# Optimization experiments

Measured on AMD Instinct MI355X. Metric: run time of the kernel, lower is better.

The kernel has to match this reference:

```python
import jax, jax.numpy as jnp
import numpy as np

N = 12000       # num nodes
E = 384000      # num edges (avg degree 32)
F_IN = 512      # num_feats
H = 64          # gnn_hid_dim (== anchor_dim)
C = 7           # num_cls
SIGMA = 1.0


def setup_inputs() -> dict:
    key = jax.random.key(0)
    ks = jax.random.split(key, 9)
    scale = lambda fan_in: 1.0 / np.sqrt(fan_in)
    return {
        "x": jax.random.normal(ks[0], (N, F_IN), dtype=jnp.float32),
        "W1": jax.random.normal(ks[1], (F_IN, H), dtype=jnp.float32) * scale(F_IN),
        "b1": jnp.zeros((H,), dtype=jnp.float32),
        "W2": jax.random.normal(ks[2], (H, H), dtype=jnp.float32) * scale(H),
        "b2": jnp.zeros((H,), dtype=jnp.float32),
        "aux": jax.random.normal(ks[3], (H,), dtype=jnp.float32),
        "clf_W": jax.random.normal(ks[4], (2 * H, C), dtype=jnp.float32) * scale(2 * H),
        "clf_b": jnp.zeros((C,), dtype=jnp.float32),
        "edge_index": jax.random.randint(ks[5], (2, E), 0, N, dtype=jnp.int64),
    }


def gcn_conv(x, W, b, src, dst, n):
    # GCNConv: D^{-1/2} (A + I) D^{-1/2} X W + b, with self-loops
    h = x @ W                                                   # [N, out]
    deg = jax.ops.segment_sum(jnp.ones(src.shape[0], h.dtype), dst,
                              num_segments=n) + 1.0             # +1 for self-loop
    inv_sqrt = jax.lax.rsqrt(deg)
    norm = inv_sqrt[src] * inv_sqrt[dst]                        # [E]
    agg = jax.ops.segment_sum(h[src] * norm[:, None], dst, num_segments=n)
    agg = agg + h / deg[:, None]                                # self-loop term (norm = 1/deg)
    return agg + b


def reference(x, W1, b1, W2, b2, aux, clf_W, clf_b, edge_index):
    src, dst = edge_index[0], edge_index[1]
    n = x.shape[0]
    h = jax.nn.relu(gcn_conv(x, W1, b1, src, dst, n))
    h = gcn_conv(h, W2, b2, src, dst, n)                        # [N, H]
    # kernel aggregate: pairwise Gaussian kernel on cosine scores
    a = aux / jnp.maximum(jnp.linalg.norm(aux), 1e-12)          # F.normalize
    hn = jnp.maximum(jnp.linalg.norm(h, axis=-1), 1e-8)         # cosine_similarity eps
    score = (h @ a) / hn                                        # [N]
    diff = score[None, :] - score[:, None]                      # [N, N]
    kappa = jnp.exp(-(diff * diff) / (SIGMA * SIGMA))           # [N, N]
    z = (kappa @ h) / jnp.sum(kappa, axis=1, keepdims=True)     # [N, H]
    return jnp.concatenate([h, z], axis=-1) @ clf_W + clf_b     # [N, C]
```

## Files before the change

kernel.cpp:

```cpp
#include <hip/hip_runtime.h>
#include <hip/hip_bf16.h>

#define N_NODES 12000
#define N_EDGES 384000
#define F_IN 512
#define H 64
#define C_CLS 7
#define KTERMS 16
#define PAD 96
#define CSTR 32
#define MOM_BLKS 192
#define NB 4
#define GEMM_BLKS 188
#define FILL_BLKS 256
#define XS_STR 68

__device__ __forceinline__ float wred_f(float x) {
    #pragma unroll
    for (int o = 32; o > 0; o >>= 1) x += __shfl_xor(x, o);
    return x;
}

__global__ __launch_bounds__(256) void init_k(int* __restrict__ cur,
                                              double* __restrict__ M,
                                              double* __restrict__ m0) {
    int i = blockIdx.x * 256 + threadIdx.x;
    if (i < N_NODES) cur[i * CSTR] = 0;
    if (i < KTERMS * 64) M[i] = 0.0;
    if (i < KTERMS) m0[i] = 0.0;
}

__global__ __launch_bounds__(256) void k1_gemm_fill(const float* __restrict__ x,
                                                    const float* __restrict__ W1,
                                                    const int* __restrict__ ei,
                                                    float* __restrict__ hbuf,
                                                    int* __restrict__ cur,
                                                    int* __restrict__ csrc) {
    const int b = blockIdx.x, t = threadIdx.x;
    if (b < GEMM_BLKS) {
        __shared__ float xs[64 * XS_STR];
        __shared__ float wsm[64 * 64];
        const int tx = t & 15, ty = t >> 4;
        const int i0 = b * 64;
        float acc[4][4] = {};
        for (int k0 = 0; k0 < F_IN; k0 += 64) {
            #pragma unroll
            for (int q = 0; q < 4; ++q) {
                int idx = t + q * 256;
                int row = idx >> 4, kg = idx & 15;
                int rg = min(i0 + row, N_NODES - 1);
                *(float4*)(&xs[row * XS_STR + kg * 4]) =
                    *(const float4*)(x + (size_t)rg * F_IN + k0 + kg * 4);
            }
            #pragma unroll
            for (int q = 0; q < 4; ++q) {
                int idx = t + q * 256;
                int r = idx >> 4, cg = idx & 15;
                *(float4*)(&wsm[r * 64 + cg * 4]) =
                    *(const float4*)(W1 + (size_t)(k0 + r) * H + cg * 4);
            }
            __syncthreads();
            #pragma unroll
            for (int kk0 = 0; kk0 < 64; kk0 += 4) {
                float4 a0 = *(const float4*)(&xs[(ty * 4 + 0) * XS_STR + kk0]);
                float4 a1 = *(const float4*)(&xs[(ty * 4 + 1) * XS_STR + kk0]);
                float4 a2 = *(const float4*)(&xs[(ty * 4 + 2) * XS_STR + kk0]);
                float4 a3 = *(const float4*)(&xs[(ty * 4 + 3) * XS_STR + kk0]);
                float4 b0 = *(const float4*)(&wsm[(kk0 + 0) * 64 + tx * 4]);
                float4 b1 = *(const float4*)(&wsm[(kk0 + 1) * 64 + tx * 4]);
                float4 b2 = *(const float4*)(&wsm[(kk0 + 2) * 64 + tx * 4]);
                float4 b3 = *(const float4*)(&wsm[(kk0 + 3) * 64 + tx * 4]);
                #define MAC4(AV, BV) \
                    acc[0][0] += AV.x * BV.x; acc[0][1] += AV.x * BV.y; \
                    acc[0][2] += AV.x * BV.z; acc[0][3] += AV.x * BV.w;
                acc[0][0] += a0.x * b0.x; acc[0][1] += a0.x * b0.y; acc[0][2] += a0.x * b0.z; acc[0][3] += a0.x * b0.w;
                acc[0][0] += a0.y * b1.x; acc[0][1] += a0.y * b1.y; acc[0][2] += a0.y * b1.z; acc[0][3] += a0.y * b1.w;
                acc[0][0] += a0.z * b2.x; acc[0][1] += a0.z * b2.y; acc[0][2] += a0.z * b2.z; acc[0][3] += a0.z * b2.w;
                acc[0][0] += a0.w * b3.x; acc[0][1] += a0.w * b3.y; acc[0][2] += a0.w * b3.z; acc[0][3] += a0.w * b3.w;
                acc[1][0] += a1.x * b0.x; acc[1][1] += a1.x * b0.y; acc[1][2] += a1.x * b0.z; acc[1][3] += a1.x * b0.w;
                acc[1][0] += a1.y * b1.x; acc[1][1] += a1.y * b1.y; acc[1][2] += a1.y * b1.z; acc[1][3] += a1.y * b1.w;
                acc[1][0] += a1.z * b2.x; acc[1][1] += a1.z * b2.y; acc[1][2] += a1.z * b2.z; acc[1][3] += a1.z * b2.w;
                acc[1][0] += a1.w * b3.x; acc[1][1] += a1.w * b3.y; acc[1][2] += a1.w * b3.z; acc[1][3] += a1.w * b3.w;
                acc[2][0] += a2.x * b0.x; acc[2][1] += a2.x * b0.y; acc[2][2] += a2.x * b0.z; acc[2][3] += a2.x * b0.w;
                acc[2][0] += a2.y * b1.x; acc[2][1] += a2.y * b1.y; acc[2][2] += a2.y * b1.z; acc[2][3] += a2.y * b1.w;
                acc[2][0] += a2.z * b2.x; acc[2][1] += a2.z * b2.y; acc[2][2] += a2.z * b2.z; acc[2][3] += a2.z * b2.w;
                acc[2][0] += a2.w * b3.x; acc[2][1] += a2.w * b3.y; acc[2][2] += a2.w * b3.z; acc[2][3] += a2.w * b3.w;
                acc[3][0] += a3.x * b0.x; acc[3][1] += a3.x * b0.y; acc[3][2] += a3.x * b0.z; acc[3][3] += a3.x * b0.w;
                acc[3][0] += a3.y * b1.x; acc[3][1] += a3.y * b1.y; acc[3][2] += a3.y * b1.z; acc[3][3] += a3.y * b1.w;
                acc[3][0] += a3.z * b2.x; acc[3][1] += a3.z * b2.y; acc[3][2] += a3.z * b2.z; acc[3][3] += a3.z * b2.w;
                acc[3][0] += a3.w * b3.x; acc[3][1] += a3.w * b3.y; acc[3][2] += a3.w * b3.z; acc[3][3] += a3.w * b3.w;
                #undef MAC4
            }
            __syncthreads();
        }
        #pragma unroll
        for (int r = 0; r < 4; ++r) {
            int row = i0 + ty * 4 + r;
            if (row < N_NODES)
                *(float4*)(hbuf + (size_t)row * H + tx * 4) =
                    make_float4(acc[r][0], acc[r][1], acc[r][2], acc[r][3]);
        }
    } else {
        for (int e = (b - GEMM_BLKS) * 256 + t; e < N_EDGES; e += FILL_BLKS * 256) {
            int s = ei[e];
            int d = ei[N_EDGES + e];
            int pos = atomicAdd(&cur[d * CSTR], 1);
            if (pos < PAD) csrc[d * PAD + pos] = s;
        }
    }
}

__global__ __launch_bounds__(256) void agg1_k(const float* __restrict__ hbuf,
                                              const float* __restrict__ b1,
                                              const int* __restrict__ cur,
                                              const int* __restrict__ csrc,
                                              float* __restrict__ h1) {
    __shared__ int2 sPair[NB * PAD];
    __shared__ int sDeg[NB];
    __shared__ float sIsd[NB];
    const int t = threadIdx.x, f = t & 63, w = t >> 6;
    const int base = blockIdx.x * NB;
    if (t < NB) {
        int d = cur[(base + t) * CSTR];
        sDeg[t] = min(d, PAD);
        sIsd[t] = rsqrtf((float)d + 1.f);
    }
    __syncthreads();
    for (int idx = t; idx < NB * PAD; idx += 256) {
        int n = idx / PAD, e = idx - n * PAD;
        if (e < sDeg[n]) {
            int s = csrc[(base + n) * PAD + e];
            float ws_ = rsqrtf((float)cur[s * CSTR] + 1.f);
            sPair[idx] = make_int2(s, __float_as_int(ws_));
        }
    }
    __syncthreads();
    const int i = base + w;
    const int deg = sDeg[w];
    const float isd = sIsd[w];
    const int2* pp = sPair + w * PAD;
    float acc = 0.f;
    int e = 0;
    for (; e + 4 <= deg; e += 4) {
        int2 p0 = pp[e], p1 = pp[e + 1], p2 = pp[e + 2], p3 = pp[e + 3];
        acc += hbuf[p0.x * H + f] * __int_as_float(p0.y)
             + hbuf[p1.x * H + f] * __int_as_float(p1.y)
             + hbuf[p2.x * H + f] * __int_as_float(p2.y)
             + hbuf[p3.x * H + f] * __int_as_float(p3.y);
    }
    for (; e < deg; ++e) {
        int2 p = pp[e];
        acc += hbuf[p.x * H + f] * __int_as_float(p.y);
    }
    float res = (acc + hbuf[i * H + f] * isd) * isd + b1[f];
    h1[i * H + f] = fmaxf(res, 0.f);
}

__global__ __launch_bounds__(256) void agg2_k(const float* __restrict__ h1,
                                              const float* __restrict__ W2,
                                              const float* __restrict__ b2,
                                              const float* __restrict__ aux,
                                              const int* __restrict__ cur,
                                              const int* __restrict__ csrc,
                                              float* __restrict__ h2,
                                              float* __restrict__ score) {
    __shared__ float w2s[64 * 64];
    __shared__ int2 sPair[NB * PAD];
    __shared__ int sDeg[NB];
    __shared__ float sIsd[NB];
    __shared__ float anorm[64];
    __shared__ float gsh[NB * 64];
    const int t = threadIdx.x, f = t & 63, w = t >> 6;
    const int base = blockIdx.x * NB;
    #pragma unroll
    for (int q = 0; q < 4; ++q) {
        int idx = t + q * 256;
        int r = idx >> 4, c4 = idx & 15;
        *(float4*)(&w2s[r * 64 + c4 * 4]) = *(const float4*)(W2 + r * H + c4 * 4);
    }
    if (t < NB) {
        int d = cur[(base + t) * CSTR];
        sDeg[t] = min(d, PAD);
        sIsd[t] = rsqrtf((float)d + 1.f);
    }
    if (t < 64) {
        float av = aux[t];
        anorm[t] = av * rsqrtf(fmaxf(wred_f(av * av), 1e-24f));
    }
    __syncthreads();
    for (int idx = t; idx < NB * PAD; idx += 256) {
        int n = idx / PAD, e = idx - n * PAD;
        if (e < sDeg[n]) {
            int s = csrc[(base + n) * PAD + e];
            float ws_ = rsqrtf((float)cur[s * CSTR] + 1.f);
            sPair[idx] = make_int2(s, __float_as_int(ws_));
        }
    }
    __syncthreads();
    const int i = base + w;
    const int deg = sDeg[w];
    const float isd = sIsd[w];
    const int2* pp = sPair + w * PAD;
    float acc = 0.f;
    int e = 0;
    for (; e + 4 <= deg; e += 4) {
        int2 p0 = pp[e], p1 = pp[e + 1], p2 = pp[e + 2], p3 = pp[e + 3];
        acc += h1[p0.x * H + f] * __int_as_float(p0.y)
             + h1[p1.x * H + f] * __int_as_float(p1.y)
             + h1[p2.x * H + f] * __int_as_float(p2.y)
             + h1[p3.x * H + f] * __int_as_float(p3.y);
    }
    for (; e < deg; ++e) {
        int2 p = pp[e];
        acc += h1[p.x * H + f] * __int_as_float(p.y);
    }
    float g = (acc + h1[i * H + f] * isd) * isd;
    gsh[w * 64 + f] = g;
    __builtin_amdgcn_wave_barrier();
    float hv = b2[f];
    #pragma unroll 16
    for (int k = 0; k < 64; ++k) hv += gsh[w * 64 + k] * w2s[k * 64 + f];
    h2[i * H + f] = hv;
    float dp = wred_f(hv * anorm[f]);
    float nn = wred_f(hv * hv);
    if (f == 0) score[i] = dp / fmaxf(sqrtf(nn), 1e-8f);
}

__global__ __launch_bounds__(256) void momden_k(const float* __restrict__ h2,
                                                const float* __restrict__ score,
                                                double* __restrict__ M,
                                                double* __restrict__ m0) {
    const int t = threadIdx.x, f = t & 63, g = t >> 6;
    float accM[KTERMS], accD[KTERMS];
    #pragma unroll
    for (int k = 0; k < KTERMS; ++k) { accM[k] = 0.f; accD[k] = 0.f; }
    for (int j = blockIdx.x * 4 + g; j < N_NODES; j += MOM_BLKS * 4) {
        float sj = score[j];
        float wj = expf(-sj * sj);
        float hv = h2[j * H + f];
        float tm = wj * hv, td = wj;
        #pragma unroll
        for (int k = 0; k < KTERMS; ++k) {
            accM[k] += tm; tm *= sj;
            accD[k] += td; td *= sj;
        }
    }
    __shared__ float Msh[4 * KTERMS * 64];
    __shared__ float Dsh[4 * KTERMS];
    #pragma unroll
    for (int k = 0; k < KTERMS; ++k) Msh[(g * KTERMS + k) * 64 + f] = accM[k];
    if (f == 0) {
        #pragma unroll
        for (int k = 0; k < KTERMS; ++k) Dsh[g * KTERMS + k] = accD[k];
    }
    __syncthreads();
    for (int idx = t; idx < KTERMS * 64; idx += 256) {
        int k = idx >> 6, ff = idx & 63;
        float sum = Msh[(0 * KTERMS + k) * 64 + ff] + Msh[(1 * KTERMS + k) * 64 + ff]
                  + Msh[(2 * KTERMS + k) * 64 + ff] + Msh[(3 * KTERMS + k) * 64 + ff];
        unsafeAtomicAdd(&M[idx], (double)sum);
    }
    if (t < KTERMS) {
        float sum = Dsh[t] + Dsh[KTERMS + t] + Dsh[2 * KTERMS + t] + Dsh[3 * KTERMS + t];
        unsafeAtomicAdd(&m0[t], (double)sum);
    }
}

__global__ __launch_bounds__(256) void final_k(const float* __restrict__ h2,
                                               const float* __restrict__ score,
                                               const double* __restrict__ M,
                                               const double* __restrict__ m0,
                                               const float* __restrict__ clfW,
                                               const float* __restrict__ clfb,
                                               float* __restrict__ out) {
    __shared__ float Ms[KTERMS * 64];
    __shared__ float m0s[KTERMS];
    __shared__ float cw[128 * C_CLS];
    __shared__ float cb[8];
    __shared__ float zh[4 * 128];
    const int t = threadIdx.x, f = t & 63, w = t >> 6;
    for (int idx = t; idx < KTERMS * 64; idx += 256) Ms[idx] = (float)M[idx];
    if (t < KTERMS) m0s[t] = (float)m0[t];
    for (int idx = t; idx < 128 * C_CLS; idx += 256) cw[idx] = clfW[idx];
    if (t < C_CLS) cb[t] = clfb[t];
    __syncthreads();
    const int base = blockIdx.x * 16;
    for (int q = 0; q < 4; ++q) {
        int i = base + q * 4 + w;
        float s = score[i];
        float c = expf(-s * s);
        float t2 = 2.f * s;
        float num = 0.f, den = 0.f;
        #pragma unroll
        for (int k = 0; k < KTERMS; ++k) {
            num += c * Ms[k * 64 + f];
            den += c * m0s[k];
            c *= t2 * (1.0f / (float)(k + 1));
        }
        zh[w * 128 + f] = h2[i * H + f];
        zh[w * 128 + 64 + f] = num / den;
        __builtin_amdgcn_wave_barrier();
        if (f < C_CLS) {
            float o = cb[f];
            #pragma unroll 8
            for (int u = 0; u < 128; ++u) o += zh[w * 128 + u] * cw[u * C_CLS + f];
            out[(size_t)i * C_CLS + f] = o;
        }
        __builtin_amdgcn_wave_barrier();
    }
}

extern "C" void kernel_launch(void* const* d_in, const int* in_sizes, int n_in,
                              void* d_out, int out_size, void* d_ws, size_t ws_size,
                              hipStream_t stream) {
    (void)in_sizes; (void)n_in; (void)out_size; (void)ws_size;
    const float* x    = (const float*)d_in[0];
    const float* W1   = (const float*)d_in[1];
    const float* b1   = (const float*)d_in[2];
    const float* W2   = (const float*)d_in[3];
    const float* b2   = (const float*)d_in[4];
    const float* aux  = (const float*)d_in[5];
    const float* clfW = (const float*)d_in[6];
    const float* clfb = (const float*)d_in[7];
    const int*   ei   = (const int*)d_in[8];
    float* out = (float*)d_out;
    char* ws = (char*)d_ws;

    float*  hbuf  = (float*)(ws + 0);
    float*  h1    = (float*)(ws + 3072000);
    float*  h2    = (float*)(ws + 6144000);
    float*  score = (float*)(ws + 9216000);
    int*    csrc  = (int*)  (ws + 9264000);
    int*    cur   = (int*)  (ws + 13872000);
    double* M     = (double*)(ws + 15408000);
    double* m0    = (double*)(ws + 15416192);

    init_k<<<47, 256, 0, stream>>>(cur, M, m0);
    k1_gemm_fill<<<GEMM_BLKS + FILL_BLKS, 256, 0, stream>>>(x, W1, ei, hbuf, cur, csrc);
    agg1_k<<<N_NODES / NB, 256, 0, stream>>>(hbuf, b1, cur, csrc, h1);
    agg2_k<<<N_NODES / NB, 256, 0, stream>>>(h1, W2, b2, aux, cur, csrc, h2, score);
    momden_k<<<MOM_BLKS, 256, 0, stream>>>(h2, score, M, m0);
    final_k<<<750, 256, 0, stream>>>(h2, score, M, m0, clfW, clfb, out);
}
```

Before: 96.48 us.

## Fuse pipeline stages into persistent megakernel with software grid barriers

```diff
diff --git a/kernel.cpp b/kernel.cpp
--- a/kernel.cpp
+++ b/kernel.cpp
@@ -9,10 +9,11 @@
 #define KTERMS 16
 #define PAD 96
 #define CSTR 32
+#define NBLK 640
+#define GEMM_BLKS 188
+#define FILL_BLKS (NBLK - GEMM_BLKS)
 #define MOM_BLKS 192
 #define NB 4
-#define GEMM_BLKS 188
-#define FILL_BLKS 256
 #define XS_STR 68
 
 __device__ __forceinline__ float wred_f(float x) {
@@ -21,25 +22,62 @@
     return x;
 }
 
+__device__ __forceinline__ void stc(float* p, float v) {
+    __hip_atomic_store(p, v, __ATOMIC_RELAXED, __HIP_MEMORY_SCOPE_AGENT);
+}
+
+__device__ __forceinline__ void gsync(int* bar, int gen) {
+    __syncthreads();
+    if (threadIdx.x == 0) {
+        const int s = blockIdx.x & 7;
+        int pos = __hip_atomic_fetch_add(&bar[s * 32], 1, __ATOMIC_RELAXED,
+                                         __HIP_MEMORY_SCOPE_AGENT);
+        if (pos == 80 * gen - 1) {
+            int r = __hip_atomic_fetch_add(&bar[320], 1, __ATOMIC_RELAXED,
+                                           __HIP_MEMORY_SCOPE_AGENT);
+            if (r == 8 * gen - 1) {
+                #pragma unroll
+                for (int k = 0; k < 8; ++k)
+                    __hip_atomic_store(&bar[512 + k * 32], gen, __ATOMIC_RELAXED,
+                                       __HIP_MEMORY_SCOPE_AGENT);
+            }
+        }
+        while (__hip_atomic_load(&bar[512 + s * 32], __ATOMIC_RELAXED,
+                                 __HIP_MEMORY_SCOPE_AGENT) < gen)
+            __builtin_amdgcn_s_sleep(8);
+        asm volatile("" ::: "memory");
+    }
+    __syncthreads();
+}
+
 __global__ __launch_bounds__(256) void init_k(int* __restrict__ cur,
                                               double* __restrict__ M,
-                                              double* __restrict__ m0) {
+                                              double* __restrict__ m0,
+                                              int* __restrict__ bar) {
     int i = blockIdx.x * 256 + threadIdx.x;
     if (i < N_NODES) cur[i * CSTR] = 0;
     if (i < KTERMS * 64) M[i] = 0.0;
     if (i < KTERMS) m0[i] = 0.0;
-}
-
-__global__ __launch_bounds__(256) void k1_gemm_fill(const float* __restrict__ x,
-                                                    const float* __restrict__ W1,
-                                                    const int* __restrict__ ei,
-                                                    float* __restrict__ hbuf,
-                                                    int* __restrict__ cur,
-                                                    int* __restrict__ csrc) {
+    if (i < 768) bar[i] = 0;
+}
+
+__global__ __launch_bounds__(256, 4) void mega_k(
+        const float* __restrict__ x, const float* __restrict__ W1,
+        const float* __restrict__ b1, const float* __restrict__ W2,
+        const float* __restrict__ b2, const float* __restrict__ aux,
+        const float* __restrict__ clfW, const float* __restrict__ clfb,
+        const int* __restrict__ ei,
+        float* __restrict__ hbuf, float* __restrict__ h1, float* __restrict__ h2,
+        float* __restrict__ score, int* __restrict__ csrc, int* __restrict__ cur,
+        double* __restrict__ M, double* __restrict__ m0, int* __restrict__ bar,
+        float* __restrict__ out) {
+    __shared__ __align__(16) char smem[33792];
     const int b = blockIdx.x, t = threadIdx.x;
+    const int f = t & 63, w = t >> 6;
+
     if (b < GEMM_BLKS) {
-        __shared__ float xs[64 * XS_STR];
-        __shared__ float wsm[64 * 64];
+        float* xs  = (float*)smem;
+        float* wsm = (float*)(smem + 17408);
         const int tx = t & 15, ty = t >> 4;
         const int i0 = b * 64;
         float acc[4][4] = {};
@@ -67,246 +105,237 @@
                 float4 a2 = *(const float4*)(&xs[(ty * 4 + 2) * XS_STR + kk0]);
                 float4 a3 = *(const float4*)(&xs[(ty * 4 + 3) * XS_STR + kk0]);
                 float4 b0 = *(const float4*)(&wsm[(kk0 + 0) * 64 + tx * 4]);
-                float4 b1 = *(const float4*)(&wsm[(kk0 + 1) * 64 + tx * 4]);
-                float4 b2 = *(const float4*)(&wsm[(kk0 + 2) * 64 + tx * 4]);
-                float4 b3 = *(const float4*)(&wsm[(kk0 + 3) * 64 + tx * 4]);
-                #define MAC4(AV, BV) \
-                    acc[0][0] += AV.x * BV.x; acc[0][1] += AV.x * BV.y; \
-                    acc[0][2] += AV.x * BV.z; acc[0][3] += AV.x * BV.w;
-                acc[0][0] += a0.x * b0.x; acc[0][1] += a0.x * b0.y; acc[0][2] += a0.x * b0.z; acc[0][3] += a0.x * b0.w;
-                acc[0][0] += a0.y * b1.x; acc[0][1] += a0.y * b1.y; acc[0][2] += a0.y * b1.z; acc[0][3] += a0.y * b1.w;
-                acc[0][0] += a0.z * b2.x; acc[0][1] += a0.z * b2.y; acc[0][2] += a0.z * b2.z; acc[0][3] += a0.z * b2.w;
-                acc[0][0] += a0.w * b3.x; acc[0][1] += a0.w * b3.y; acc[0][2] += a0.w * b3.z; acc[0][3] += a0.w * b3.w;
-                acc[1][0] += a1.x * b0.x; acc[1][1] += a1.x * b0.y; acc[1][2] += a1.x * b0.z; acc[1][3] += a1.x * b0.w;
-                acc[1][0] += a1.y * b1.x; acc[1][1] += a1.y * b1.y; acc[1][2] += a1.y * b1.z; acc[1][3] += a1.y * b1.w;
-                acc[1][0] += a1.z * b2.x; acc[1][1] += a1.z * b2.y; acc[1][2] += a1.z * b2.z; acc[1][3] += a1.z * b2.w;
-                acc[1][0] += a1.w * b3.x; acc[1][1] += a1.w * b3.y; acc[1][2] += a1.w * b3.z; acc[1][3] += a1.w * b3.w;
-                acc[2][0] += a2.x * b0.x; acc[2][1] += a2.x * b0.y; acc[2][2] += a2.x * b0.z; acc[2][3] += a2.x * b0.w;
-                acc[2][0] += a2.y * b1.x; acc[2][1] += a2.y * b1.y; acc[2][2] += a2.y * b1.z; acc[2][3] += a2.y * b1.w;
-                acc[2][0] += a2.z * b2.x; acc[2][1] += a2.z * b2.y; acc[2][2] += a2.z * b2.z; acc[2][3] += a2.z * b2.w;
-                acc[2][0] += a2.w * b3.x; acc[2][1] += a2.w * b3.y; acc[2][2] += a2.w * b3.z; acc[2][3] += a2.w * b3.w;
-                acc[3][0] += a3.x * b0.x; acc[3][1] += a3.x * b0.y; acc[3][2] += a3.x * b0.z; acc[3][3] += a3.x * b0.w;
-                acc[3][0] += a3.y * b1.x; acc[3][1] += a3.y * b1.y; acc[3][2] += a3.y * b1.z; acc[3][3] += a3.y * b1.w;
-                acc[3][0] += a3.z * b2.x; acc[3][1] += a3.z * b2.y; acc[3][2] += a3.z * b2.z; acc[3][3] += a3.z * b2.w;
-                acc[3][0] += a3.w * b3.x; acc[3][1] += a3.w * b3.y; acc[3][2] += a3.w * b3.z; acc[3][3] += a3.w * b3.w;
-                #undef MAC4
+                float4 b1v = *(const float4*)(&wsm[(kk0 + 1) * 64 + tx * 4]);
+                float4 b2v = *(const float4*)(&wsm[(kk0 + 2) * 64 + tx * 4]);
+                float4 b3v = *(const float4*)(&wsm[(kk0 + 3) * 64 + tx * 4]);
+                acc[0][0] += a0.x * b0.x;  acc[0][1] += a0.x * b0.y;  acc[0][2] += a0.x * b0.z;  acc[0][3] += a0.x * b0.w;
+                acc[0][0] += a0.y * b1v.x; acc[0][1] += a0.y * b1v.y; acc[0][2] += a0.y * b1v.z; acc[0][3] += a0.y * b1v.w;
+                acc[0][0] += a0.z * b2v.x; acc[0][1] += a0.z * b2v.y; acc[0][2] += a0.z * b2v.z; acc[0][3] += a0.z * b2v.w;
+                acc[0][0] += a0.w * b3v.x; acc[0][1] += a0.w * b3v.y; acc[0][2] += a0.w * b3v.z; acc[0][3] += a0.w * b3v.w;
+                acc[1][0] += a1.x * b0.x;  acc[1][1] += a1.x * b0.y;  acc[1][2] += a1.x * b0.z;  acc[1][3] += a1.x * b0.w;
+                acc[1][0] += a1.y * b1v.x; acc[1][1] += a1.y * b1v.y; acc[1][2] += a1.y * b1v.z; acc[1][3] += a1.y * b1v.w;
+                acc[1][0] += a1.z * b2v.x; acc[1][1] += a1.z * b2v.y; acc[1][2] += a1.z * b2v.z; acc[1][3] += a1.z * b2v.w;
+                acc[1][0] += a1.w * b3v.x; acc[1][1] += a1.w * b3v.y; acc[1][2] += a1.w * b3v.z; acc[1][3] += a1.w * b3v.w;
+                acc[2][0] += a2.x * b0.x;  acc[2][1] += a2.x * b0.y;  acc[2][2] += a2.x * b0.z;  acc[2][3] += a2.x * b0.w;
+                acc[2][0] += a2.y * b1v.x; acc[2][1] += a2.y * b1v.y; acc[2][2] += a2.y * b1v.z; acc[2][3] += a2.y * b1v.w;
+                acc[2][0] += a2.z * b2v.x; acc[2][1] += a2.z * b2v.y; acc[2][2] += a2.z * b2v.z; acc[2][3] += a2.z * b2v.w;
+                acc[2][0] += a2.w * b3v.x; acc[2][1] += a2.w * b3v.y; acc[2][2] += a2.w * b3v.z; acc[2][3] += a2.w * b3v.w;
+                acc[3][0] += a3.x * b0.x;  acc[3][1] += a3.x * b0.y;  acc[3][2] += a3.x * b0.z;  acc[3][3] += a3.x * b0.w;
+                acc[3][0] += a3.y * b1v.x; acc[3][1] += a3.y * b1v.y; acc[3][2] += a3.y * b1v.z; acc[3][3] += a3.y * b1v.w;
+                acc[3][0] += a3.z * b2v.x; acc[3][1] += a3.z * b2v.y; acc[3][2] += a3.z * b2v.z; acc[3][3] += a3.z * b2v.w;
+                acc[3][0] += a3.w * b3v.x; acc[3][1] += a3.w * b3v.y; acc[3][2] += a3.w * b3v.z; acc[3][3] += a3.w * b3v.w;
             }
             __syncthreads();
         }
         #pragma unroll
         for (int r = 0; r < 4; ++r) {
             int row = i0 + ty * 4 + r;
-            if (row < N_NODES)
-                *(float4*)(hbuf + (size_t)row * H + tx * 4) =
-                    make_float4(acc[r][0], acc[r][1], acc[r][2], acc[r][3]);
+            if (row < N_NODES) {
+                stc(&hbuf[(size_t)row * H + tx * 4 + 0], acc[r][0]);
+                stc(&hbuf[(size_t)row * H + tx * 4 + 1], acc[r][1]);
+                stc(&hbuf[(size_t)row * H + tx * 4 + 2], acc[r][2]);
+                stc(&hbuf[(size_t)row * H + tx * 4 + 3], acc[r][3]);
+            }
         }
     } else {
         for (int e = (b - GEMM_BLKS) * 256 + t; e < N_EDGES; e += FILL_BLKS * 256) {
             int s = ei[e];
             int d = ei[N_EDGES + e];
-            int pos = atomicAdd(&cur[d * CSTR], 1);
-            if (pos < PAD) csrc[d * PAD + pos] = s;
-        }
-    }
-}
-
-__global__ __launch_bounds__(256) void agg1_k(const float* __restrict__ hbuf,
-                                              const float* __restrict__ b1,
-                                              const int* __restrict__ cur,
-                                              const int* __restrict__ csrc,
-                                              float* __restrict__ h1) {
-    __shared__ int2 sPair[NB * PAD];
-    __shared__ int sDeg[NB];
-    __shared__ float sIsd[NB];
-    const int t = threadIdx.x, f = t & 63, w = t >> 6;
-    const int base = blockIdx.x * NB;
-    if (t < NB) {
-        int d = cur[(base + t) * CSTR];
-        sDeg[t] = min(d, PAD);
-        sIsd[t] = rsqrtf((float)d + 1.f);
-    }
-    __syncthreads();
-    for (int idx = t; idx < NB * PAD; idx += 256) {
-        int n = idx / PAD, e = idx - n * PAD;
-        if (e < sDeg[n]) {
-            int s = csrc[(base + n) * PAD + e];
-            float ws_ = rsqrtf((float)cur[s * CSTR] + 1.f);
-            sPair[idx] = make_int2(s, __float_as_int(ws_));
-        }
-    }
-    __syncthreads();
-    const int i = base + w;
-    const int deg = sDeg[w];
-    const float isd = sIsd[w];
-    const int2* pp = sPair + w * PAD;
-    float acc = 0.f;
-    int e = 0;
-    for (; e + 4 <= deg; e += 4) {
-        int2 p0 = pp[e], p1 = pp[e + 1], p2 = pp[e + 2], p3 = pp[e + 3];
-        acc += hbuf[p0.x * H + f] * __int_as_float(p0.y)
-             + hbuf[p1.x * H + f] * __int_as_float(p1.y)
-             + hbuf[p2.x * H + f] * __int_as_float(p2.y)
-             + hbuf[p3.x * H + f] * __int_as_float(p3.y);
-    }
-    for (; e < deg; ++e) {
-        int2 p = pp[e];
-        acc += hbuf[p.x * H + f] * __int_as_float(p.y);
-    }
-    float res = (acc + hbuf[i * H + f] * isd) * isd + b1[f];
-    h1[i * H + f] = fmaxf(res, 0.f);
-}
-
-__global__ __launch_bounds__(256) void agg2_k(const float* __restrict__ h1,
-                                              const float* __restrict__ W2,
-                                              const float* __restrict__ b2,
-                                              const float* __restrict__ aux,
-                                              const int* __restrict__ cur,
-                                              const int* __restrict__ csrc,
-                                              float* __restrict__ h2,
-                                              float* __restrict__ score) {
-    __shared__ float w2s[64 * 64];
-    __shared__ int2 sPair[NB * PAD];
-    __shared__ int sDeg[NB];
-    __shared__ float sIsd[NB];
-    __shared__ float anorm[64];
-    __shared__ float gsh[NB * 64];
-    const int t = threadIdx.x, f = t & 63, w = t >> 6;
-    const int base = blockIdx.x * NB;
-    #pragma unroll
-    for (int q = 0; q < 4; ++q) {
-        int idx = t + q * 256;
-        int r = idx >> 4, c4 = idx & 15;
-        *(float4*)(&w2s[r * 64 + c4 * 4]) = *(const float4*)(W2 + r * H + c4 * 4);
-    }
-    if (t < NB) {
-        int d = cur[(base + t) * CSTR];
-        sDeg[t] = min(d, PAD);
-        sIsd[t] = rsqrtf((float)d + 1.f);
-    }
-    if (t < 64) {
-        float av = aux[t];
-        anorm[t] = av * rsqrtf(fmaxf(wred_f(av * av), 1e-24f));
-    }
-    __syncthreads();
-    for (int idx = t; idx < NB * PAD; idx += 256) {
-        int n = idx / PAD, e = idx - n * PAD;
-        if (e < sDeg[n]) {
-            int s = csrc[(base + n) * PAD + e];
-            float ws_ = rsqrtf((float)cur[s * CSTR] + 1.f);
-            sPair[idx] = make_int2(s, __float_as_int(ws_));
-        }
-    }
-    __syncthreads();
-    const int i = base + w;
-    const int deg = sDeg[w];
-    const float isd = sIsd[w];
-    const int2* pp = sPair + w * PAD;
-    float acc = 0.f;
-    int e = 0;
-    for (; e + 4 <= deg; e += 4) {
-        int2 p0 = pp[e], p1 = pp[e + 1], p2 = pp[e + 2], p3 = pp[e + 3];
-        acc += h1[p0.x * H + f] * __int_as_float(p0.y)
-             + h1[p1.x * H + f] * __int_as_float(p1.y)
-             + h1[p2.x * H + f] * __int_as_float(p2.y)
-             + h1[p3.x * H + f] * __int_as_float(p3.y);
-    }
-    for (; e < deg; ++e) {
-        int2 p = pp[e];
-        acc += h1[p.x * H + f] * __int_as_float(p.y);
-    }
-    float g = (acc + h1[i * H + f] * isd) * isd;
-    gsh[w * 64 + f] = g;
-    __builtin_amdgcn_wave_barrier();
-    float hv = b2[f];
-    #pragma unroll 16
-    for (int k = 0; k < 64; ++k) hv += gsh[w * 64 + k] * w2s[k * 64 + f];
-    h2[i * H + f] = hv;
-    float dp = wred_f(hv * anorm[f]);
-    float nn = wred_f(hv * hv);
-    if (f == 0) score[i] = dp / fmaxf(sqrtf(nn), 1e-8f);
-}
-
-__global__ __launch_bounds__(256) void momden_k(const float* __restrict__ h2,
-                                                const float* __restrict__ score,
-                                                double* __restrict__ M,
-                                                double* __restrict__ m0) {
-    const int t = threadIdx.x, f = t & 63, g = t >> 6;
-    float accM[KTERMS], accD[KTERMS];
-    #pragma unroll
-    for (int k = 0; k < KTERMS; ++k) { accM[k] = 0.f; accD[k] = 0.f; }
-    for (int j = blockIdx.x * 4 + g; j < N_NODES; j += MOM_BLKS * 4) {
-        float sj = score[j];
-        float wj = expf(-sj * sj);
-        float hv = h2[j * H + f];
-        float tm = wj * hv, td = wj;
+            int pos = __hip_atomic_fetch_add(&cur[d * CSTR], 1, __ATOMIC_RELAXED,
+                                             __HIP_MEMORY_SCOPE_AGENT);
+            if (pos < PAD)
+                (void)__hip_atomic_exchange(&csrc[d * PAD + pos], s, __ATOMIC_RELAXED,
+                                            __HIP_MEMORY_SCOPE_AGENT);
+        }
+    }
+    gsync(bar, 1);
+
+    {
+        int2*  sPair = (int2*)smem;
+        int*   sDeg  = (int*)(smem + 3072);
+        float* sIsd  = (float*)(smem + 3088);
+        for (int g = b; g < N_NODES / NB; g += NBLK) {
+            const int base = g * NB;
+            __syncthreads();
+            if (t < NB) {
+                int d = cur[(base + t) * CSTR];
+                sDeg[t] = min(d, PAD);
+                sIsd[t] = rsqrtf((float)d + 1.f);
+            }
+            __syncthreads();
+            for (int idx = t; idx < NB * PAD; idx += 256) {
+                int n = idx / PAD, e = idx - n * PAD;
+                if (e < sDeg[n]) {
+                    int s = csrc[(base + n) * PAD + e];
+                    float ws_ = rsqrtf((float)cur[s * CSTR] + 1.f);
+                    sPair[idx] = make_int2(s, __float_as_int(ws_));
+                }
+            }
+            __syncthreads();
+            const int i = base + w;
+            const int deg = sDeg[w];
+            const float isd = sIsd[w];
+            const int2* pp = sPair + w * PAD;
+            float acc = 0.f;
+            int e = 0;
+            for (; e + 4 <= deg; e += 4) {
+                int2 p0 = pp[e], p1 = pp[e + 1], p2 = pp[e + 2], p3 = pp[e + 3];
+                acc += hbuf[p0.x * H + f] * __int_as_float(p0.y)
+                     + hbuf[p1.x * H + f] * __int_as_float(p1.y)
+                     + hbuf[p2.x * H + f] * __int_as_float(p2.y)
+                     + hbuf[p3.x * H + f] * __int_as_float(p3.y);
+            }
+            for (; e < deg; ++e) {
+                int2 p = pp[e];
+                acc += hbuf[p.x * H + f] * __int_as_float(p.y);
+            }
+            float res = (acc + hbuf[i * H + f] * isd) * isd + b1[f];
+            stc(&h1[i * H + f], fmaxf(res, 0.f));
+        }
+    }
+    gsync(bar, 2);
+
+    {
+        int2*  sPair = (int2*)smem;
+        int*   sDeg  = (int*)(smem + 3072);
+        float* sIsd  = (float*)(smem + 3088);
+        float* w2s   = (float*)(smem + 3104);
+        float* anorm = (float*)(smem + 19488);
+        float* gsh   = (float*)(smem + 19744);
         #pragma unroll
-        for (int k = 0; k < KTERMS; ++k) {
-            accM[k] += tm; tm *= sj;
-            accD[k] += td; td *= sj;
-        }
-    }
-    __shared__ float Msh[4 * KTERMS * 64];
-    __shared__ float Dsh[4 * KTERMS];
-    #pragma unroll
-    for (int k = 0; k < KTERMS; ++k) Msh[(g * KTERMS + k) * 64 + f] = accM[k];
-    if (f == 0) {
+        for (int q = 0; q < 4; ++q) {
+            int idx = t + q * 256;
+            int r = idx >> 4, c4 = idx & 15;
+            *(float4*)(&w2s[r * 64 + c4 * 4]) = *(const float4*)(W2 + r * H + c4 * 4);
+        }
+        if (t < 64) {
+            float av = aux[t];
+            anorm[t] = av * rsqrtf(fmaxf(wred_f(av * av), 1e-24f));
+        }
+        for (int g = b; g < N_NODES / NB; g += NBLK) {
+            const int base = g * NB;
+            __syncthreads();
+            if (t < NB) {
+                int d = cur[(base + t) * CSTR];
+                sDeg[t] = min(d, PAD);
+                sIsd[t] = rsqrtf((float)d + 1.f);
+            }
+            __syncthreads();
+            for (int idx = t; idx < NB * PAD; idx += 256) {
+                int n = idx / PAD, e = idx - n * PAD;
+                if (e < sDeg[n]) {
+                    int s = csrc[(base + n) * PAD + e];
+                    float ws_ = rsqrtf((float)cur[s * CSTR] + 1.f);
+                    sPair[idx] = make_int2(s, __float_as_int(ws_));
+                }
+            }
+            __syncthreads();
+            const int i = base + w;
+            const int deg = sDeg[w];
+            const float isd = sIsd[w];
+            const int2* pp = sPair + w * PAD;
+            float acc = 0.f;
+            int e = 0;
+            for (; e + 4 <= deg; e += 4) {
+                int2 p0 = pp[e], p1 = pp[e + 1], p2 = pp[e + 2], p3 = pp[e + 3];
+                acc += h1[p0.x * H + f] * __int_as_float(p0.y)
+                     + h1[p1.x * H + f] * __int_as_float(p1.y)
+                     + h1[p2.x * H + f] * __int_as_float(p2.y)
+                     + h1[p3.x * H + f] * __int_as_float(p3.y);
+            }
+            for (; e < deg; ++e) {
+                int2 p = pp[e];
+                acc += h1[p.x * H + f] * __int_as_float(p.y);
+            }
+            float gg = (acc + h1[i * H + f] * isd) * isd;
+            gsh[w * 64 + f] = gg;
+            __builtin_amdgcn_wave_barrier();
+            float hv = b2[f];
+            #pragma unroll 16
+            for (int k = 0; k < 64; ++k) hv += gsh[w * 64 + k] * w2s[k * 64 + f];
+            stc(&h2[i * H + f], hv);
+            float dp = wred_f(hv * anorm[f]);
+            float nn = wred_f(hv * hv);
+            if (f == 0) stc(&score[i], dp / fmaxf(sqrtf(nn), 1e-8f));
+            __builtin_amdgcn_wave_barrier();
+        }
+    }
+    gsync(bar, 3);
+
+    if (b < MOM_BLKS) {
+        float* Msh = (float*)smem;
+        float* Dsh = (float*)(smem + 16384);
+        float accM[KTERMS], accD[KTERMS];
         #pragma unroll
-        for (int k = 0; k < KTERMS; ++k) Dsh[g * KTERMS + k] = accD[k];
-    }
-    __syncthreads();
-    for (int idx = t; idx < KTERMS * 64; idx += 256) {
-        int k = idx >> 6, ff = idx & 63;
-        float sum = Msh[(0 * KTERMS + k) * 64 + ff] + Msh[(1 * KTERMS + k) * 64 + ff]
-                  + Msh[(2 * KTERMS + k) * 64 + ff] + Msh[(3 * KTERMS + k) * 64 + ff];
-        unsafeAtomicAdd(&M[idx], (double)sum);
-    }
-    if (t < KTERMS) {
-        float sum = Dsh[t] + Dsh[KTERMS + t] + Dsh[2 * KTERMS + t] + Dsh[3 * KTERMS + t];
-        unsafeAtomicAdd(&m0[t], (double)sum);
-    }
-}
-
-__global__ __launch_bounds__(256) void final_k(const float* __restrict__ h2,
-                                               const float* __restrict__ score,
-                                               const double* __restrict__ M,
-                                               const double* __restrict__ m0,
-                                               const float* __restrict__ clfW,
-                                               const float* __restrict__ clfb,
-                                               float* __restrict__ out) {
-    __shared__ float Ms[KTERMS * 64];
-    __shared__ float m0s[KTERMS];
-    __shared__ float cw[128 * C_CLS];
-    __shared__ float cb[8];
-    __shared__ float zh[4 * 128];
-    const int t = threadIdx.x, f = t & 63, w = t >> 6;
-    for (int idx = t; idx < KTERMS * 64; idx += 256) Ms[idx] = (float)M[idx];
-    if (t < KTERMS) m0s[t] = (float)m0[t];
-    for (int idx = t; idx < 128 * C_CLS; idx += 256) cw[idx] = clfW[idx];
-    if (t < C_CLS) cb[t] = clfb[t];
-    __syncthreads();
-    const int base = blockIdx.x * 16;
-    for (int q = 0; q < 4; ++q) {
-        int i = base + q * 4 + w;
-        float s = score[i];
-        float c = expf(-s * s);
-        float t2 = 2.f * s;
-        float num = 0.f, den = 0.f;
+        for (int k = 0; k < KTERMS; ++k) { accM[k] = 0.f; accD[k] = 0.f; }
+        for (int j = b * 4 + w; j < N_NODES; j += MOM_BLKS * 4) {
+            float sj = score[j];
+            float wj = expf(-sj * sj);
+            float hv = h2[j * H + f];
+            float tm = wj * hv, td = wj;
+            #pragma unroll
+            for (int k = 0; k < KTERMS; ++k) {
+                accM[k] += tm; tm *= sj;
+                accD[k] += td; td *= sj;
+            }
+        }
         #pragma unroll
-        for (int k = 0; k < KTERMS; ++k) {
-            num += c * Ms[k * 64 + f];
-            den += c * m0s[k];
-            c *= t2 * (1.0f / (float)(k + 1));
-        }
-        zh[w * 128 + f] = h2[i * H + f];
-        zh[w * 128 + 64 + f] = num / den;
-        __builtin_amdgcn_wave_barrier();
-        if (f < C_CLS) {
-            float o = cb[f];
-            #pragma unroll 8
-            for (int u = 0; u < 128; ++u) o += zh[w * 128 + u] * cw[u * C_CLS + f];
-            out[(size_t)i * C_CLS + f] = o;
-        }
-        __builtin_amdgcn_wave_barrier();
+        for (int k = 0; k < KTERMS; ++k) Msh[(w * KTERMS + k) * 64 + f] = accM[k];
+        if (f == 0) {
+            #pragma unroll
+            for (int k = 0; k < KTERMS; ++k) Dsh[w * KTERMS + k] = accD[k];
+        }
+        __syncthreads();
+        for (int idx = t; idx < KTERMS * 64; idx += 256) {
+            int k = idx >> 6, ff = idx & 63;
+            float sum = Msh[(0 * KTERMS + k) * 64 + ff] + Msh[(1 * KTERMS + k) * 64 + ff]
+                      + Msh[(2 * KTERMS + k) * 64 + ff] + Msh[(3 * KTERMS + k) * 64 + ff];
+            unsafeAtomicAdd(&M[idx], (double)sum);
+        }
+        if (t < KTERMS) {
+            float sum = Dsh[t] + Dsh[KTERMS + t] + Dsh[2 * KTERMS + t] + Dsh[3 * KTERMS + t];
+            unsafeAtomicAdd(&m0[t], (double)sum);
+        }
+    }
+    gsync(bar, 4);
+
+    {
+        float* Ms  = (float*)smem;
+        float* m0s = (float*)(smem + 4096);
+        float* cw  = (float*)(smem + 4160);
+        float* cb  = (float*)(smem + 7744);
+        float* zh  = (float*)(smem + 7776);
+        for (int idx = t; idx < KTERMS * 64; idx += 256) Ms[idx] = (float)M[idx];
+        if (t < KTERMS) m0s[t] = (float)m0[t];
+        for (int idx = t; idx < 128 * C_CLS; idx += 256) cw[idx] = clfW[idx];
+        if (t < C_CLS) cb[t] = clfb[t];
+        __syncthreads();
+        for (int g = b; g < 750; g += NBLK) {
+            const int base = g * 16;
+            for (int q = 0; q < 4; ++q) {
+                int i = base + q * 4 + w;
+                float s = score[i];
+                float c = expf(-s * s);
+                float t2 = 2.f * s;
+                float num = 0.f, den = 0.f;
+                #pragma unroll
+                for (int k = 0; k < KTERMS; ++k) {
+                    num += c * Ms[k * 64 + f];
+                    den += c * m0s[k];
+                    c *= t2 * (1.0f / (float)(k + 1));
+                }
+                zh[w * 128 + f] = h2[i * H + f];
+                zh[w * 128 + 64 + f] = num / den;
+                __builtin_amdgcn_wave_barrier();
+                if (f < C_CLS) {
+                    float o = cb[f];
+                    #pragma unroll 8
+                    for (int u = 0; u < 128; ++u) o += zh[w * 128 + u] * cw[u * C_CLS + f];
+                    out[(size_t)i * C_CLS + f] = o;
+                }
+                __builtin_amdgcn_wave_barrier();
+            }
+        }
     }
 }
 
@@ -334,11 +363,9 @@
     int*    cur   = (int*)  (ws + 13872000);
     double* M     = (double*)(ws + 15408000);
     double* m0    = (double*)(ws + 15416192);
-
-    init_k<<<47, 256, 0, stream>>>(cur, M, m0);
-    k1_gemm_fill<<<GEMM_BLKS + FILL_BLKS, 256, 0, stream>>>(x, W1, ei, hbuf, cur, csrc);
-    agg1_k<<<N_NODES / NB, 256, 0, stream>>>(hbuf, b1, cur, csrc, h1);
-    agg2_k<<<N_NODES / NB, 256, 0, stream>>>(h1, W2, b2, aux, cur, csrc, h2, score);
-    momden_k<<<MOM_BLKS, 256, 0, stream>>>(h2, score, M, m0);
-    final_k<<<750, 256, 0, stream>>>(h2, score, M, m0, clfW, clfb, out);
-}
+    int*    bar   = (int*)  (ws + 15416320);
+
+    init_k<<<47, 256, 0, stream>>>(cur, M, m0, bar);
+    mega_k<<<NBLK, 256, 0, stream>>>(x, W1, b1, W2, b2, aux, clfW, clfb, ei,
+                                     hbuf, h1, h2, score, csrc, cur, M, m0, bar, out);
+}
```

Result: slower. 149.1 us (+54.6%).
